# Kernel tuning notes

Hardware: AMD Instinct MI355X
Metric: run time of the kernel (lower is better)

The kernel has to match this reference:

```python
import jax, jax.numpy as jnp
import numpy as np
from jax import lax


def _conv2d_same(x, w, b):
    # NHWC input, HWIO kernel, stride 1, SAME padding (matches keras Conv2D)
    y = lax.conv_general_dilated(x, w, window_strides=(1, 1), padding='SAME',
                                 dimension_numbers=('NHWC', 'HWIO', 'NHWC'))
    return y + b


def setup_inputs() -> dict:
    key = jax.random.key(0)
    k1, k2, k3, k4 = jax.random.split(key, 4)
    B, H, W, C = 16, 128, 128, 256
    F = 256
    inputs = jax.random.normal(k1, (B, H, W, C), dtype=jnp.float32)
    # offset conv: small random weights so offsets are non-trivial but in-range-ish
    w_off = jax.random.normal(k2, (3, 3, C, 2), dtype=jnp.float32) * 0.05
    b_off = jnp.zeros((2,), dtype=jnp.float32)
    w_def = jax.random.normal(k3, (3, 3, C, F), dtype=jnp.float32) * (1.0 / np.sqrt(9 * C))
    b_def = jax.random.normal(k4, (F,), dtype=jnp.float32) * 0.01
    return {"inputs": inputs, "w_off": w_off, "b_off": b_off,
            "w_def": w_def, "b_def": b_def}


def reference(inputs, w_off, b_off, w_def, b_def):
    B, H, W, C = inputs.shape
    # 1) predict per-pixel (dy, dx) offsets
    offsets = _conv2d_same(inputs, w_off, b_off)          # (B,H,W,2)
    off_h = offsets[..., 0]                               # (B,H,W)
    off_w = offsets[..., 1]                               # (B,H,W)
    # 2) build sampling grid, add offsets, clip, truncate to int (tf.cast semantics;
    #    values are non-negative after clip so truncation == floor)
    yy, xx = jnp.meshgrid(jnp.arange(H, dtype=inputs.dtype),
                          jnp.arange(W, dtype=inputs.dtype), indexing='ij')
    y = jnp.clip(yy[None] + off_h, 0.0, H - 1).astype(jnp.int32)   # (B,H,W)
    x = jnp.clip(xx[None] + off_w, 0.0, W - 1).astype(jnp.int32)   # (B,H,W)
    # 3) gather: one offset per pixel, shared across all channels
    lin = (y * W + x).reshape(B, H * W, 1)                # (B,HW,1)
    sampled = jnp.take_along_axis(inputs.reshape(B, H * W, C), lin, axis=1)
    sampled = sampled.reshape(B, H, W, C)
    # 4) main conv on resampled features
    return _conv2d_same(sampled, w_def, b_def)
```

## Files before the change

kernel.cpp:

```cpp
#include <hip/hip_runtime.h>
#include <hip/hip_bf16.h>

typedef __attribute__((ext_vector_type(8))) short bf16x8;
typedef __attribute__((ext_vector_type(4))) float f32x4;

__device__ __forceinline__ unsigned short f2bf(float f) {
  __hip_bfloat16 h = __float2bfloat16(f);
  return *reinterpret_cast<unsigned short*>(&h);
}

__device__ __forceinline__ void gld_lds16(void* lds, const void* g) {
  __builtin_amdgcn_global_load_lds(
      (const __attribute__((address_space(1))) unsigned int*)g,
      (__attribute__((address_space(3))) unsigned int*)lds, 16, 0, 0);
}

__global__ __launch_bounds__(256) void k1_offs_gather(
    const float* __restrict__ in, const float* __restrict__ w_off,
    const float* __restrict__ b_off, unsigned short* __restrict__ samp) {
  __shared__ float tile[3][128][34];
  __shared__ float wlf[9 * 64];
  __shared__ double dsum[2][128][2];
  __shared__ int lin_lds[128];

  const int bid = blockIdx.x;
  const int b = bid >> 7, h = bid & 127;
  const int t = threadIdx.x;
  const int w = t & 127, half = t >> 7, ch0 = half * 16;

  double a0 = 0.0, a1 = 0.0;

  for (int c0 = 0; c0 < 256; c0 += 32) {
    __syncthreads();
    for (int i = t; i < 576; i += 256) {
      int tap = i >> 6, r = i & 63;
      wlf[i] = w_off[tap * 512 + c0 * 2 + r];
    }
    for (int dr = 0; dr < 3; ++dr) {
      int hh = h + dr - 1;
      if ((unsigned)hh < 128u) {
        const float* rbase = in + ((size_t)(b * 128 + hh) * 128) * 256 + c0;
        #pragma unroll
        for (int it = 0; it < 4; ++it) {
          int idx = it * 256 + t;
          int ww = idx >> 3, cq = idx & 7;
          const float4 v = *(const float4*)(rbase + ww * 256 + cq * 4);
          float* dst = &tile[dr][ww][cq * 4];
          *(float2*)dst = make_float2(v.x, v.y);
          *(float2*)(dst + 2) = make_float2(v.z, v.w);
        }
      } else {
        #pragma unroll
        for (int it = 0; it < 4; ++it) {
          int idx = it * 256 + t;
          int ww = idx >> 3, cq = idx & 7;
          float* dst = &tile[dr][ww][cq * 4];
          *(float2*)dst = make_float2(0.f, 0.f);
          *(float2*)(dst + 2) = make_float2(0.f, 0.f);
        }
      }
    }
    __syncthreads();
    #pragma unroll
    for (int dr = 0; dr < 3; ++dr) {
      #pragma unroll
      for (int dc = 0; dc < 3; ++dc) {
        int wsrc = w + dc - 1;
        if ((unsigned)wsrc >= 128u) continue;
        const float2* tp2 = (const float2*)&tile[dr][wsrc][ch0];
        const float2* wp2 = (const float2*)&wlf[(dr * 3 + dc) * 64 + ch0 * 2];
        #pragma unroll
        for (int c2 = 0; c2 < 8; ++c2) {
          float2 v = tp2[c2];
          float2 wa = wp2[2 * c2];
          float2 wb = wp2[2 * c2 + 1];
          a0 += (double)v.x * (double)wa.x;
          a1 += (double)v.x * (double)wa.y;
          a0 += (double)v.y * (double)wb.x;
          a1 += (double)v.y * (double)wb.y;
        }
      }
    }
  }
  dsum[half][w][0] = a0;
  dsum[half][w][1] = a1;
  __syncthreads();
  if (t < 128) {
    double o0 = dsum[0][t][0] + dsum[1][t][0] + (double)b_off[0];
    double o1 = dsum[0][t][1] + dsum[1][t][1] + (double)b_off[1];
    double yd = (double)h + o0;
    double xd = (double)t + o1;
    yd = yd < 0.0 ? 0.0 : (yd > 127.0 ? 127.0 : yd);
    xd = xd < 0.0 ? 0.0 : (xd > 127.0 ? 127.0 : xd);
    int y = (int)yd, x = (int)xd;
    lin_lds[t] = y * 128 + x;
  }
  __syncthreads();
  const float* imgbase = in + (size_t)b * 16384 * 256;
  unsigned short* obase = samp + (size_t)bid * 128 * 256;
  for (int it = 0; it < 32; ++it) {
    int idx = it * 256 + t;
    int px = idx >> 6, cv = idx & 63;
    const float4 v = *(const float4*)(imgbase + (size_t)lin_lds[px] * 256 + cv * 4);
    ushort4 o;
    o.x = f2bf(v.x); o.y = f2bf(v.y); o.z = f2bf(v.z); o.w = f2bf(v.w);
    *(ushort4*)(obase + px * 256 + cv * 4) = o;
  }
}

__global__ __launch_bounds__(256) void k2_wT(const float* __restrict__ wdef,
                                             unsigned short* __restrict__ wT) {
  int g = blockIdx.x * 256 + threadIdx.x;
  int tap = g >> 16;
  int n = (g >> 8) & 255;
  int k = g & 255;
  wT[g] = f2bf(wdef[((size_t)tap * 256 + k) * 256 + n]);
}

struct Frags { bf16x8 a[8]; bf16x8 b[4]; };

__global__ __launch_bounds__(512, 2) void k3_conv(
    const unsigned short* __restrict__ samp, const unsigned short* __restrict__ wT,
    const float* __restrict__ b_def, float* __restrict__ out,
    const unsigned short* __restrict__ zerobuf) {
  __shared__ __align__(16) unsigned char smem[131072];

  const int bid0 = blockIdx.x;
  const int mt = (bid0 & 7) * 128 + (bid0 >> 3);
  const int bimg = mt >> 6;
  const int h0 = (mt & 63) * 2;

  const int tid = threadIdx.x;
  const int lane = tid & 63, wave = tid >> 6;
  const int wr = wave >> 2, wc = wave & 3;
  const int r15 = lane & 15, g4 = lane >> 4;
  const int g4eff = g4 ^ ((r15 >> 1) & 3);

  const char* sA = (const char*)smem + (wr * 128 + r15) * 64 + g4eff * 16;
  const char* sB = (const char*)smem + 65536 + (wc * 64 + r15) * 64 + g4eff * 16;

  const int chq = tid & 3;
  const int pix = tid >> 2;
  const int chs = chq ^ ((pix >> 1) & 3);
  const unsigned short* pA[2];
  const unsigned short* pB[2];
  unsigned vmask[2];
  #pragma unroll
  for (int it = 0; it < 2; ++it) {
    const int hh = h0 + it;
    pA[it] = samp + ((size_t)(bimg * 128 + hh) * 128 + pix) * 256 + chs * 8;
    pB[it] = wT + (size_t)(it * 128 + pix) * 256 + chs * 8;
    unsigned m = 0;
    #pragma unroll
    for (int tap = 0; tap < 9; ++tap) {
      const int dr = tap / 3 - 1, dc = tap % 3 - 1;
      if ((unsigned)(hh + dr) < 128u && (unsigned)(pix + dc) < 128u)
        m |= 1u << tap;
    }
    vmask[it] = m;
  }
  const unsigned short* zb = zerobuf + chq * 8;

  f32x4 acc[8][4];
  #pragma unroll
  for (int i = 0; i < 8; ++i)
    #pragma unroll
    for (int j = 0; j < 4; ++j) acc[i][j] = (f32x4){0.f, 0.f, 0.f, 0.f};

  auto stage = [&](int ts, int SLOT) {
    const int tap = ts >> 3, kc = ts & 7;
    const int q = (tap * 11) >> 5;
    const int tapdelta = ((q - 1) * 128 + (tap - q * 3 - 1)) * 256 + kc * 32;
    const int boffg = tap * 65536 + kc * 32;
    unsigned char* Ad = smem + SLOT * 16384;
    unsigned char* Bd = smem + 65536 + SLOT * 16384;
    #pragma unroll
    for (int it = 0; it < 2; ++it)
      gld_lds16(Bd + (it * 512 + tid) * 16, pB[it] + boffg);
    #pragma unroll
    for (int it = 0; it < 2; ++it) {
      const unsigned short* src =
          ((vmask[it] >> tap) & 1) ? (pA[it] + tapdelta) : zb;
      gld_lds16(Ad + (it * 512 + tid) * 16, src);
    }
  };

  auto readfr = [&](Frags& f, int SLOT) {
    #pragma unroll
    for (int ni = 0; ni < 4; ++ni)
      f.b[ni] = *(const bf16x8*)(sB + SLOT * 16384 + ni * 1024);
    #pragma unroll
    for (int mi = 0; mi < 8; ++mi)
      f.a[mi] = *(const bf16x8*)(sA + SLOT * 16384 + mi * 1024);
  };

  auto launder = [&](Frags& f) {
    #pragma unroll
    for (int i = 0; i < 8; ++i) asm volatile("" : "+v"(f.a[i]));
    #pragma unroll
    for (int i = 0; i < 4; ++i) asm volatile("" : "+v"(f.b[i]));
  };

  auto mfma32 = [&](Frags& f) {
    #pragma unroll
    for (int mi = 0; mi < 8; ++mi)
      #pragma unroll
      for (int ni = 0; ni < 4; ++ni)
        acc[mi][ni] = __builtin_amdgcn_mfma_f32_16x16x32_bf16(
            f.a[mi], f.b[ni], acc[mi][ni], 0, 0, 0);
  };

  Frags fr0, fr1;

#define K3_STEP(T_RT, SLOT_NXT, FR_CUR, FR_NXT, DO_READS, DO_STAGE, VMSTR) \
  {                                                                        \
    asm volatile("s_waitcnt lgkmcnt(0)" ::: "memory");                     \
    launder(FR_CUR);                                                       \
    __builtin_amdgcn_sched_barrier(0);                                     \
    __builtin_amdgcn_s_setprio(1);                                         \
    if (DO_READS) readfr(FR_NXT, SLOT_NXT);                                \
    if (DO_STAGE) stage((T_RT) + 3, ((SLOT_NXT) + 2) & 3);                 \
    mfma32(FR_CUR);                                                        \
    if (DO_READS && DO_STAGE) {                                            \
      _Pragma("unroll")                                                    \
      for (int u = 0; u < 4; ++u) {                                        \
        __builtin_amdgcn_sched_group_barrier(0x008, 8, 0);                 \
        __builtin_amdgcn_sched_group_barrier(0x100, 3, 0);                 \
        __builtin_amdgcn_sched_group_barrier(0x030, 1, 0);                 \
      }                                                                    \
    }                                                                      \
    __builtin_amdgcn_s_setprio(0);                                         \
    __builtin_amdgcn_sched_barrier(0);                                     \
    asm volatile("s_waitcnt " VMSTR ::: "memory");                         \
    __builtin_amdgcn_s_barrier();                                          \
    asm volatile("" ::: "memory");                                         \
  }

  stage(0, 0); stage(1, 1); stage(2, 2);
  asm volatile("s_waitcnt vmcnt(4)" ::: "memory");
  __builtin_amdgcn_s_barrier();
  asm volatile("" ::: "memory");
  readfr(fr0, 0);

  for (int tb = 0; tb < 68; tb += 4) {
    K3_STEP(tb + 0, 1, fr0, fr1, true, true, "vmcnt(4)");
    K3_STEP(tb + 1, 2, fr1, fr0, true, true, "vmcnt(4)");
    K3_STEP(tb + 2, 3, fr0, fr1, true, true, "vmcnt(4)");
    K3_STEP(tb + 3, 0, fr1, fr0, true, true, "vmcnt(4)");
  }
  K3_STEP(68, 1, fr0, fr1, true, true,  "vmcnt(4)");
  K3_STEP(69, 2, fr1, fr0, true, false, "vmcnt(0)");
  K3_STEP(70, 3, fr0, fr1, true, false, "vmcnt(0)");
  {
    asm volatile("s_waitcnt lgkmcnt(0)" ::: "memory");
    launder(fr1);
    __builtin_amdgcn_sched_barrier(0);
    mfma32(fr1);
  }
#undef K3_STEP

  const int colg = wc * 64 + r15;
  float bias[4];
  #pragma unroll
  for (int ni = 0; ni < 4; ++ni) bias[ni] = b_def[colg + ni * 16];
  #pragma unroll
  for (int mi = 0; mi < 8; ++mi) {
    const int r0 = wr * 128 + mi * 16 + g4 * 4;
    #pragma unroll
    for (int j = 0; j < 4; ++j) {
      float* orow = out + ((size_t)mt * 256 + r0 + j) * 256 + colg;
      #pragma unroll
      for (int ni = 0; ni < 4; ++ni) orow[ni * 16] = acc[mi][ni][j] + bias[ni];
    }
  }
}

extern "C" void kernel_launch(void* const* d_in, const int* in_sizes, int n_in,
                              void* d_out, int out_size, void* d_ws, size_t ws_size,
                              hipStream_t stream) {
  const float* in = (const float*)d_in[0];
  const float* w_off = (const float*)d_in[1];
  const float* b_off = (const float*)d_in[2];
  const float* w_def = (const float*)d_in[3];
  const float* b_def = (const float*)d_in[4];
  float* out = (float*)d_out;

  char* ws = (char*)d_ws;
  unsigned short* zerobuf = (unsigned short*)ws;
  unsigned short* wT = (unsigned short*)(ws + 4096);
  unsigned short* samp = (unsigned short*)(ws + 4096 + 1179648);

  hipMemsetAsync(ws, 0, 4096, stream);
  hipLaunchKernelGGL(k2_wT, dim3(2304), dim3(256), 0, stream, w_def, wT);
  hipLaunchKernelGGL(k1_offs_gather, dim3(2048), dim3(256), 0, stream,
                     in, w_off, b_off, samp);
  hipLaunchKernelGGL(k3_conv, dim3(1024), dim3(512), 0, stream,
                     samp, wT, b_def, out, zerobuf);
}
```

Before: 492.7 us.

## Compute offset conv for four rows per block to reuse halo rows

The offset-conv-plus-gather kernel now handles four output rows per block instead of one. It loads a six-row input tile over 16-channel chunks, so each input row is read about 1.5 times instead of 3. Each thread accumulates two output pixels over the full channel range, which removes the cross-half double reduction. The trade-off is a grid shrunk from 2048 to 512 blocks, a longer serial gather loop per block, and possibly more FP64 register pressure.

New measurement: 496.4 us. About the same (+0.8%).

```diff
diff --git a/kernel.cpp b/kernel.cpp
--- a/kernel.cpp
+++ b/kernel.cpp
@@ -18,93 +18,84 @@
 __global__ __launch_bounds__(256) void k1_offs_gather(
     const float* __restrict__ in, const float* __restrict__ w_off,
     const float* __restrict__ b_off, unsigned short* __restrict__ samp) {
-  __shared__ float tile[3][128][34];
-  __shared__ float wlf[9 * 64];
-  __shared__ double dsum[2][128][2];
-  __shared__ int lin_lds[128];
+  __shared__ float tile[6][128][17];
+  __shared__ float wlf[288];
+  __shared__ int lin_lds[512];
 
   const int bid = blockIdx.x;
-  const int b = bid >> 7, h = bid & 127;
+  const int b = bid >> 5, h0 = (bid & 31) << 2;
   const int t = threadIdx.x;
-  const int w = t & 127, half = t >> 7, ch0 = half * 16;
-
-  double a0 = 0.0, a1 = 0.0;
-
-  for (int c0 = 0; c0 < 256; c0 += 32) {
+
+  const int r_[2] = {t >> 7, 2 + (t >> 7)};
+  const int px_ = t & 127;
+
+  double aY[2] = {0.0, 0.0}, aX[2] = {0.0, 0.0};
+
+  for (int c0 = 0; c0 < 256; c0 += 16) {
     __syncthreads();
-    for (int i = t; i < 576; i += 256) {
-      int tap = i >> 6, r = i & 63;
-      wlf[i] = w_off[tap * 512 + c0 * 2 + r];
-    }
-    for (int dr = 0; dr < 3; ++dr) {
-      int hh = h + dr - 1;
-      if ((unsigned)hh < 128u) {
-        const float* rbase = in + ((size_t)(b * 128 + hh) * 128) * 256 + c0;
+    for (int i = t; i < 288; i += 256) {
+      const int tap = i >> 5, r = i & 31;
+      wlf[i] = w_off[tap * 512 + (c0 + (r >> 1)) * 2 + (r & 1)];
+    }
+    #pragma unroll
+    for (int it = 0; it < 12; ++it) {
+      const int idx = it * 256 + t;
+      const int row = idx >> 9;
+      const int rest = idx & 511;
+      const int px = rest >> 2, c4 = rest & 3;
+      const int hh = h0 - 1 + row;
+      float4 v = make_float4(0.f, 0.f, 0.f, 0.f);
+      if ((unsigned)hh < 128u)
+        v = *(const float4*)(in + ((size_t)(b * 128 + hh) * 128 + px) * 256 +
+                             c0 + c4 * 4);
+      float* dst = &tile[row][px][c4 * 4];
+      dst[0] = v.x; dst[1] = v.y; dst[2] = v.z; dst[3] = v.w;
+    }
+    __syncthreads();
+    #pragma unroll
+    for (int pi = 0; pi < 2; ++pi) {
+      const int r = r_[pi];
+      #pragma unroll
+      for (int tap = 0; tap < 9; ++tap) {
+        const int dr = tap / 3, dc = tap % 3 - 1;
+        const int wsrc = px_ + dc;
+        if ((unsigned)wsrc >= 128u) continue;
+        const float* tp = &tile[r + dr][wsrc][0];
+        const float2* w2 = (const float2*)&wlf[tap * 32];
         #pragma unroll
-        for (int it = 0; it < 4; ++it) {
-          int idx = it * 256 + t;
-          int ww = idx >> 3, cq = idx & 7;
-          const float4 v = *(const float4*)(rbase + ww * 256 + cq * 4);
-          float* dst = &tile[dr][ww][cq * 4];
-          *(float2*)dst = make_float2(v.x, v.y);
-          *(float2*)(dst + 2) = make_float2(v.z, v.w);
-        }
-      } else {
-        #pragma unroll
-        for (int it = 0; it < 4; ++it) {
-          int idx = it * 256 + t;
-          int ww = idx >> 3, cq = idx & 7;
-          float* dst = &tile[dr][ww][cq * 4];
-          *(float2*)dst = make_float2(0.f, 0.f);
-          *(float2*)(dst + 2) = make_float2(0.f, 0.f);
+        for (int c = 0; c < 16; ++c) {
+          const double v = (double)tp[c];
+          const float2 w = w2[c];
+          aY[pi] += v * (double)w.x;
+          aX[pi] += v * (double)w.y;
         }
       }
     }
-    __syncthreads();
-    #pragma unroll
-    for (int dr = 0; dr < 3; ++dr) {
-      #pragma unroll
-      for (int dc = 0; dc < 3; ++dc) {
-        int wsrc = w + dc - 1;
-        if ((unsigned)wsrc >= 128u) continue;
-        const float2* tp2 = (const float2*)&tile[dr][wsrc][ch0];
-        const float2* wp2 = (const float2*)&wlf[(dr * 3 + dc) * 64 + ch0 * 2];
-        #pragma unroll
-        for (int c2 = 0; c2 < 8; ++c2) {
-          float2 v = tp2[c2];
-          float2 wa = wp2[2 * c2];
-          float2 wb = wp2[2 * c2 + 1];
-          a0 += (double)v.x * (double)wa.x;
-          a1 += (double)v.x * (double)wa.y;
-          a0 += (double)v.y * (double)wb.x;
-          a1 += (double)v.y * (double)wb.y;
-        }
-      }
-    }
-  }
-  dsum[half][w][0] = a0;
-  dsum[half][w][1] = a1;
-  __syncthreads();
-  if (t < 128) {
-    double o0 = dsum[0][t][0] + dsum[1][t][0] + (double)b_off[0];
-    double o1 = dsum[0][t][1] + dsum[1][t][1] + (double)b_off[1];
-    double yd = (double)h + o0;
-    double xd = (double)t + o1;
-    yd = yd < 0.0 ? 0.0 : (yd > 127.0 ? 127.0 : yd);
-    xd = xd < 0.0 ? 0.0 : (xd > 127.0 ? 127.0 : xd);
-    int y = (int)yd, x = (int)xd;
-    lin_lds[t] = y * 128 + x;
+  }
+  {
+    const double b0 = (double)b_off[0], b1 = (double)b_off[1];
+    #pragma unroll
+    for (int pi = 0; pi < 2; ++pi) {
+      const int h = h0 + r_[pi];
+      double yd = (double)h + (aY[pi] + b0);
+      double xd = (double)px_ + (aX[pi] + b1);
+      yd = yd < 0.0 ? 0.0 : (yd > 127.0 ? 127.0 : yd);
+      xd = xd < 0.0 ? 0.0 : (xd > 127.0 ? 127.0 : xd);
+      lin_lds[pi * 256 + t] = ((int)yd) * 128 + (int)xd;
+    }
   }
   __syncthreads();
   const float* imgbase = in + (size_t)b * 16384 * 256;
-  unsigned short* obase = samp + (size_t)bid * 128 * 256;
-  for (int it = 0; it < 32; ++it) {
-    int idx = it * 256 + t;
-    int px = idx >> 6, cv = idx & 63;
-    const float4 v = *(const float4*)(imgbase + (size_t)lin_lds[px] * 256 + cv * 4);
+  unsigned short* obase = samp + ((size_t)(b * 128 + h0)) * 128 * 256;
+  #pragma unroll 4
+  for (int it = 0; it < 128; ++it) {
+    const int idx = it * 256 + t;
+    const int p = idx >> 6, cv = idx & 63;
+    const float4 v =
+        *(const float4*)(imgbase + (size_t)lin_lds[p] * 256 + cv * 4);
     ushort4 o;
     o.x = f2bf(v.x); o.y = f2bf(v.y); o.z = f2bf(v.z); o.w = f2bf(v.w);
-    *(ushort4*)(obase + px * 256 + cv * 4) = o;
+    *(ushort4*)(obase + (size_t)p * 256 + cv * 4) = o;
   }
 }
 
@@ -292,7 +283,7 @@
 
   hipMemsetAsync(ws, 0, 4096, stream);
   hipLaunchKernelGGL(k2_wT, dim3(2304), dim3(256), 0, stream, w_def, wT);
-  hipLaunchKernelGGL(k1_offs_gather, dim3(2048), dim3(256), 0, stream,
+  hipLaunchKernelGGL(k1_offs_gather, dim3(512), dim3(256), 0, stream,
                      in, w_off, b_off, samp);
   hipLaunchKernelGGL(k3_conv, dim3(1024), dim3(512), 0, stream,
                      samp, wT, b_def, out, zerobuf);
```
